# Kernel tuning notes

Measured on AMD Instinct MI355X. Metric: run time of the kernel, lower is better.

The kernel has to match this reference:

```python
import jax, jax.numpy as jnp
import numpy as np

L, H, P = 16384, 1024, 512  # seq len, model width, state size (conj_sym: P = ssm_size//2)
DT_MIN, DT_MAX = 1e-3, 1e-1
STEP_RESCALE = 1.0


def setup_inputs() -> dict:
    key = jax.random.key(0)
    ks = jax.random.split(key, 7)
    input_sequence = jax.random.normal(ks[0], (L, H), dtype=jnp.float32)
    # Lambda: stable diagonal (Re < 0), like DPLR-HiPPO (Re = -0.5, spread imag parts)
    Lambda_re = -0.5 - jax.random.uniform(ks[1], (P,), dtype=jnp.float32)
    Lambda_im = 10.0 * jax.random.normal(ks[2], (P,), dtype=jnp.float32)
    # B (P,H,2) and C (H,P,2): real/imag stacked parameterization
    B = jax.random.normal(ks[3], (P, H, 2), dtype=jnp.float32) / np.float32(np.sqrt(H))
    C = jax.random.normal(ks[4], (H, P, 2), dtype=jnp.float32) / np.float32(np.sqrt(P))
    D = jax.random.normal(ks[5], (H,), dtype=jnp.float32)
    log_step = (jax.random.uniform(ks[6], (P, 1), dtype=jnp.float32)
                * (np.log(DT_MAX) - np.log(DT_MIN)) + np.log(DT_MIN)).astype(jnp.float32)
    return {"input_sequence": input_sequence, "Lambda_re": Lambda_re,
            "Lambda_im": Lambda_im, "B": B, "C": C, "D": D, "log_step": log_step}


def _binop(q_i, q_j):
    # diagonal linear recurrence composition; elementwise, so works on stacked arrays
    A_i, b_i = q_i
    A_j, b_j = q_j
    return (A_j * A_i, A_j * b_i + b_j)


def reference(input_sequence, Lambda_re, Lambda_im, B, C, D, log_step):
    Lambda = Lambda_re + 1j * Lambda_im                      # (P,) complex64
    B_tilde = B[..., 0] + 1j * B[..., 1]                     # (P,H)
    C_tilde = C[..., 0] + 1j * C[..., 1]                     # (H,P)
    Delta = STEP_RESCALE * jnp.exp(log_step[:, 0])           # (P,)
    # ZOH discretization
    Lambda_bar = jnp.exp(Lambda * Delta)                     # (P,)
    B_bar = ((Lambda_bar - 1.0) / Lambda)[:, None] * B_tilde # (P,H)
    # per-step scan elements
    Lambda_elements = jnp.broadcast_to(Lambda_bar, (input_sequence.shape[0], P))
    Bu_elements = jnp.einsum('lh,ph->lp', input_sequence, B_bar)  # (L,P) complex
    _, xs = jax.lax.associative_scan(_binop, (Lambda_elements, Bu_elements))
    # conj_sym readout: 2 * Re(C x)
    ys = 2.0 * jnp.einsum('lp,hp->lh', xs, C_tilde).real     # (L,H) float32
    return ys + input_sequence * D
```

## Files before the change

### kernel.cpp

```cpp
#include <hip/hip_runtime.h>
#include <math.h>

#define LL 16384
#define HH 1024
#define PP 512
#define NP2 1024
#define CHUNK 64
#define NCHUNK 256
#define BM 128
#define BN 128
#define BK 64

typedef unsigned short u16;
typedef __attribute__((ext_vector_type(8))) short bf16x8;
typedef __attribute__((ext_vector_type(4))) float f32x4;

__device__ __forceinline__ u16 f2bf(float f) {
    unsigned u = __float_as_uint(f);
    unsigned r = 0x7fffu + ((u >> 16) & 1u);
    return (u16)((u + r) >> 16);
}
__device__ __forceinline__ float bf2f(u16 x) {
    return __uint_as_float(((unsigned)x) << 16);
}

__device__ __forceinline__ void gload_lds16(const void* g, void* l) {
    __builtin_amdgcn_global_load_lds(
        (const __attribute__((address_space(1))) unsigned int*)g,
        (__attribute__((address_space(3))) unsigned int*)l, 16, 0, 0);
}

__global__ void k_setup(const float* __restrict__ lre, const float* __restrict__ lim,
                        const float* __restrict__ logstep,
                        float* __restrict__ gre, float* __restrict__ gim,
                        float* __restrict__ lbre, float* __restrict__ lbim,
                        float* __restrict__ ltre, float* __restrict__ ltim) {
    int p = threadIdx.x;
    if (p >= PP) return;
    float dt = expf(logstep[p]);
    float ar = lre[p], ai = lim[p];
    float e = expf(ar * dt);
    float s, c;
    sincosf(ai * dt, &s, &c);
    float Lr = e * c, Li = e * s;
    lbre[p] = Lr; lbim[p] = Li;
    float nr = Lr - 1.0f, ni = Li;
    float den = ar * ar + ai * ai;
    gre[p] = (nr * ar + ni * ai) / den;
    gim[p] = (ni * ar - nr * ai) / den;
    float tr = Lr, ti = Li;
    for (int i = 0; i < 6; i++) {
        float rr = tr * tr - ti * ti;
        float mm = 2.0f * tr * ti;
        tr = rr; ti = mm;
    }
    ltre[p] = tr; ltim[p] = ti;
}

__global__ void k_prep2(const float* __restrict__ B,
                        const float* __restrict__ gre, const float* __restrict__ gim,
                        const float* __restrict__ C,
                        u16* __restrict__ bb, u16* __restrict__ cp) {
    if (blockIdx.x < 2048) {
        int t = blockIdx.x * 256 + threadIdx.x;
        int p = t >> 10, h = t & 1023;
        float2 b = ((const float2*)B)[t];
        float gr = gre[p], gi = gim[p];
        bb[(size_t)(2 * p) * HH + h]     = f2bf(gr * b.x - gi * b.y);
        bb[(size_t)(2 * p + 1) * HH + h] = f2bf(gr * b.y + gi * b.x);
    } else {
        int t = (blockIdx.x - 2048) * 256 + threadIdx.x;
        int h = t >> 9, p = t & 511;
        float2 c = ((const float2*)C)[t];
        cp[(size_t)h * NP2 + 2 * p]     = f2bf(c.x);
        cp[(size_t)h * NP2 + 2 * p + 1] = f2bf(-c.y);
    }
}

__global__ void k_cvt(const float* __restrict__ s, u16* __restrict__ d) {
    size_t i = ((size_t)blockIdx.x * 256 + threadIdx.x) * 4;
    float4 v = *(const float4*)&s[i];
    unsigned lo = (unsigned)f2bf(v.x) | ((unsigned)f2bf(v.y) << 16);
    unsigned hi = (unsigned)f2bf(v.z) | ((unsigned)f2bf(v.w) << 16);
    *(uint2*)&d[i] = make_uint2(lo, hi);
}

template<int FUSE>
__global__ __launch_bounds__(256) void k_gemm(
        const u16* __restrict__ A, const u16* __restrict__ Bt,
        void* __restrict__ outp, const int K,
        const u16* __restrict__ ubf, const float* __restrict__ Din,
        const float* __restrict__ lbre, const float* __restrict__ lbim,
        float* __restrict__ frO, float* __restrict__ fiO) {
    __shared__ u16 smem[2 * BM * BK];
    u16* lA = smem;
    u16* lB = smem + BM * BK;
    const int b = blockIdx.x;
    const int xcd = b & 7, s = b >> 3;
    const int m0 = (xcd * 16 + (s >> 3)) * BM;
    const int n0 = (s & 7) * BN;
    const int N = 8 * BN;
    const int t = threadIdx.x;
    const int lane = t & 63, wid = t >> 6;
    const int wm = (wid >> 1) * 64, wn = (wid & 1) * 64;
    const int frow = lane & 15, quad = lane >> 4;
    const int swz = frow & 7;

    f32x4 acc[4][4];
    #pragma unroll
    for (int i = 0; i < 4; i++)
        #pragma unroll
        for (int j = 0; j < 4; j++) acc[i][j] = (f32x4){0.f, 0.f, 0.f, 0.f};

    const int sr = t >> 3, slot = t & 7;
    const int seg = slot ^ (sr & 7);
    const u16* gA = A + (size_t)(m0 + sr) * K + seg * 8;
    const u16* gB = Bt + (size_t)(n0 + sr) * K + seg * 8;
    u16* dA = &lA[sr * BK + slot * 8];
    u16* dB = &lB[sr * BK + slot * 8];

    for (int k0 = 0; k0 < K; k0 += BK) {
        __syncthreads();
        #pragma unroll
        for (int g = 0; g < 4; g++) {
            gload_lds16(gA + (size_t)(32 * g) * K + k0, dA + 32 * g * BK);
            gload_lds16(gB + (size_t)(32 * g) * K + k0, dB + 32 * g * BK);
        }
        __syncthreads();
        #pragma unroll
        for (int kk = 0; kk < 2; kk++) {
            bf16x8 av[4], bv[4];
            #pragma unroll
            for (int i = 0; i < 4; i++)
                av[i] = *(const bf16x8*)&lA[(wm + i * 16 + frow) * BK
                                            + (((kk << 2) | quad) ^ swz) * 8];
            #pragma unroll
            for (int j = 0; j < 4; j++)
                bv[j] = *(const bf16x8*)&lB[(wn + j * 16 + frow) * BK
                                            + (((kk << 2) | quad) ^ swz) * 8];
            #pragma unroll
            for (int i = 0; i < 4; i++)
                #pragma unroll
                for (int j = 0; j < 4; j++)
                    acc[i][j] = __builtin_amdgcn_mfma_f32_16x16x32_bf16(
                        av[i], bv[j], acc[i][j], 0, 0, 0);
        }
    }

    if (FUSE) {
        float* Cout = (float*)outp;
        #pragma unroll
        for (int i = 0; i < 4; i++) {
            const int row = m0 + wm + i * 16 + quad * 4;
            #pragma unroll
            for (int j = 0; j < 4; j++) {
                const int col = n0 + wn + j * 16 + frow;
                const float dv = Din[col];
                f32x4 v = acc[i][j];
                #pragma unroll
                for (int r = 0; r < 4; r++) {
                    const size_t o = (size_t)(row + r) * N + col;
                    Cout[o] = 2.0f * v[r] + bf2f(ubf[o]) * dv;
                }
            }
        }
    } else {
        u16* Cb = (u16*)outp;
        unsigned* sm32 = (unsigned*)smem;
        const int half = wm >> 6;
        const int sq = t & 63, sh = t >> 6;
        const int sp = (n0 >> 1) + sq;
        float sar = 0.f, sai = 0.f, sxr = 0.f, sxi = 0.f;
        if (t < 128) { sar = lbre[sp]; sai = lbim[sp]; }
        __syncthreads();
        #pragma unroll
        for (int i = 0; i < 4; i++) {
            #pragma unroll
            for (int j = 0; j < 4; j++) {
                f32x4 v = acc[i][j];
                #pragma unroll
                for (int r = 0; r < 4; r++)
                    smem[half * 2048 + (quad * 4 + r) * 128 + wn + j * 16 + frow]
                        = f2bf(v[r]);
            }
            __syncthreads();
            #pragma unroll
            for (int c = 0; c < 2; c++) {
                const int fe = (t + c * 256) * 8;
                const int hh = fe >> 11, rem = fe & 2047;
                const int qr = rem >> 7, cb = rem & 127;
                const int row = m0 + hh * 64 + i * 16 + qr;
                *(uint4*)&Cb[(size_t)row * N + n0 + cb] = *(const uint4*)&smem[fe];
            }
            if (t < 128) {
                #pragma unroll
                for (int r = 0; r < 16; r++) {
                    unsigned v = sm32[sh * 1024 + r * 64 + sq];
                    float br = bf2f((u16)(v & 0xffff));
                    float bi = bf2f((u16)(v >> 16));
                    float nr = sar * sxr - sai * sxi + br;
                    float ni = sar * sxi + sai * sxr + bi;
                    sxr = nr; sxi = ni;
                }
            }
            __syncthreads();
        }
        if (t < 128) {
            const int chunk = (m0 >> 6) + sh;
            frO[chunk * PP + sp] = sxr;
            fiO[chunk * PP + sp] = sxi;
        }
    }
}

__global__ __launch_bounds__(256) void k_scan2(
        const float* __restrict__ fr, const float* __restrict__ fi,
        const float* __restrict__ ltre, const float* __restrict__ ltim,
        float* __restrict__ cr, float* __restrict__ ci) {
    __shared__ float Ar[NCHUNK], Ai[NCHUNK], br[NCHUNK], bi[NCHUNK];
    const int p = blockIdx.x;
    const int c = threadIdx.x;
    const float lr = ltre[p], li = ltim[p];
    Ar[c] = lr; Ai[c] = li;
    br[c] = fr[c * PP + p];
    bi[c] = fi[c * PP + p];
    __syncthreads();
    #pragma unroll
    for (int d = 1; d < NCHUNK; d <<= 1) {
        float pAr = 0.f, pAi = 0.f, pbr = 0.f, pbi = 0.f;
        const bool has = (c >= d);
        if (has) { pAr = Ar[c-d]; pAi = Ai[c-d]; pbr = br[c-d]; pbi = bi[c-d]; }
        float cAr = Ar[c], cAi = Ai[c], cbr = br[c], cbi = bi[c];
        __syncthreads();
        if (has) {
            Ar[c] = cAr * pAr - cAi * pAi;
            Ai[c] = cAr * pAi + cAi * pAr;
            br[c] = cAr * pbr - cAi * pbi + cbr;
            bi[c] = cAr * pbi + cAi * pbr + cbi;
        }
        __syncthreads();
    }
    cr[c * PP + p] = (c == 0) ? 0.f : br[c-1];
    ci[c * PP + p] = (c == 0) ? 0.f : bi[c-1];
}

__global__ void k_scan3(unsigned* __restrict__ bu,
                        const float* __restrict__ lbre, const float* __restrict__ lbim,
                        const float* __restrict__ cr, const float* __restrict__ ci) {
    int p = blockIdx.x * 256 + threadIdx.x;
    int c = blockIdx.y;
    float ar = lbre[p], ai = lbim[p];
    float xr = cr[c * PP + p], xi = ci[c * PP + p];
    unsigned* b = bu + (size_t)c * CHUNK * PP + p;
    for (int j = 0; j < CHUNK; j++) {
        unsigned v = *b;
        float br = bf2f((u16)(v & 0xffff));
        float bi = bf2f((u16)(v >> 16));
        float nr = ar * xr - ai * xi + br;
        float ni = ar * xi + ai * xr + bi;
        xr = nr; xi = ni;
        *b = (unsigned)f2bf(xr) | ((unsigned)f2bf(xi) << 16);
        b += PP;
    }
}

extern "C" void kernel_launch(void* const* d_in, const int* in_sizes, int n_in,
                              void* d_out, int out_size, void* d_ws, size_t ws_size,
                              hipStream_t stream) {
    const float* u       = (const float*)d_in[0];
    const float* lre     = (const float*)d_in[1];
    const float* lim     = (const float*)d_in[2];
    const float* B       = (const float*)d_in[3];
    const float* C       = (const float*)d_in[4];
    const float* D       = (const float*)d_in[5];
    const float* logstep = (const float*)d_in[6];
    float* out = (float*)d_out;

    float* w = (float*)d_ws;
    float* gre  = w;
    float* gim  = w + 512;
    float* lbre = w + 1024;
    float* lbim = w + 1536;
    float* ltre = w + 2048;
    float* ltim = w + 2560;
    float* fr   = w + 4096;
    float* fi   = fr + NCHUNK * PP;
    float* cr   = fi + NCHUNK * PP;
    float* ci   = cr + NCHUNK * PP;
    u16*   bub  = (u16*)(w + (1 << 20));
    u16*   ub   = bub + (size_t)LL * NP2;
    u16*   bb   = ub + (size_t)LL * HH;
    u16*   cp   = bb + (size_t)NP2 * HH;

    k_setup<<<1, 512, 0, stream>>>(lre, lim, logstep, gre, gim, lbre, lbim, ltre, ltim);
    k_prep2<<<4096, 256, 0, stream>>>(B, gre, gim, C, bb, cp);
    k_cvt<<<(LL * HH) / 1024, 256, 0, stream>>>(u, ub);
    k_gemm<0><<<(NP2 / BN) * (LL / BM), 256, 0, stream>>>(
        ub, bb, bub, HH, nullptr, nullptr, lbre, lbim, fr, fi);
    k_scan2<<<PP, NCHUNK, 0, stream>>>(fr, fi, ltre, ltim, cr, ci);
    k_scan3<<<dim3(PP / 256, NCHUNK), 256, 0, stream>>>(
        (unsigned*)bub, lbre, lbim, cr, ci);
    k_gemm<1><<<(HH / BN) * (LL / BM), 256, 0, stream>>>(
        bub, cp, out, NP2, ub, D, nullptr, nullptr, nullptr, nullptr);
}
```

Before: 251.6 us.

## Rewrite GEMMs with 256x256 tiles, 4-stage async LDS pipeline, batched scan loads

```diff
diff --git a/kernel.cpp b/kernel.cpp
--- a/kernel.cpp
+++ b/kernel.cpp
@@ -7,9 +7,11 @@
 #define NP2 1024
 #define CHUNK 64
 #define NCHUNK 256
-#define BM 128
-#define BN 128
-#define BK 64
+
+#define BM2 256
+#define BN2 256
+#define SUBK 32
+#define REG_U16 16384
 
 typedef unsigned short u16;
 typedef __attribute__((ext_vector_type(8))) short bf16x8;
@@ -86,71 +88,80 @@
 }
 
 template<int FUSE>
-__global__ __launch_bounds__(256) void k_gemm(
+__global__ __launch_bounds__(512, 2) void k_gemm2(
         const u16* __restrict__ A, const u16* __restrict__ Bt,
         void* __restrict__ outp, const int K,
         const u16* __restrict__ ubf, const float* __restrict__ Din,
         const float* __restrict__ lbre, const float* __restrict__ lbim,
         float* __restrict__ frO, float* __restrict__ fiO) {
-    __shared__ u16 smem[2 * BM * BK];
-    u16* lA = smem;
-    u16* lB = smem + BM * BK;
+    extern __shared__ u16 smem[];
     const int b = blockIdx.x;
-    const int xcd = b & 7, s = b >> 3;
-    const int m0 = (xcd * 16 + (s >> 3)) * BM;
-    const int n0 = (s & 7) * BN;
-    const int N = 8 * BN;
+    const int xcd = b & 7, sidx = b >> 3;
+    const int m0 = (xcd * 8 + (sidx >> 2)) * BM2;
+    const int n0 = (sidx & 3) * BN2;
     const int t = threadIdx.x;
     const int lane = t & 63, wid = t >> 6;
-    const int wm = (wid >> 1) * 64, wn = (wid & 1) * 64;
-    const int frow = lane & 15, quad = lane >> 4;
-    const int swz = frow & 7;
-
-    f32x4 acc[4][4];
+    const int wm = (wid >> 2) * 128, wn = (wid & 3) * 64;
+    const int frow = lane & 15, quad = (lane >> 4) & 3;
+
+    f32x4 acc[8][4];
     #pragma unroll
-    for (int i = 0; i < 4; i++)
+    for (int i = 0; i < 8; i++)
         #pragma unroll
         for (int j = 0; j < 4; j++) acc[i][j] = (f32x4){0.f, 0.f, 0.f, 0.f};
 
-    const int sr = t >> 3, slot = t & 7;
-    const int seg = slot ^ (sr & 7);
+    const int sr = t >> 2, slot = t & 3;
+    const int seg = slot ^ (sr & 3);
     const u16* gA = A + (size_t)(m0 + sr) * K + seg * 8;
     const u16* gB = Bt + (size_t)(n0 + sr) * K + seg * 8;
-    u16* dA = &lA[sr * BK + slot * 8];
-    u16* dB = &lB[sr * BK + slot * 8];
-
-    for (int k0 = 0; k0 < K; k0 += BK) {
-        __syncthreads();
-        #pragma unroll
-        for (int g = 0; g < 4; g++) {
-            gload_lds16(gA + (size_t)(32 * g) * K + k0, dA + 32 * g * BK);
-            gload_lds16(gB + (size_t)(32 * g) * K + k0, dB + 32 * g * BK);
-        }
-        __syncthreads();
-        #pragma unroll
-        for (int kk = 0; kk < 2; kk++) {
-            bf16x8 av[4], bv[4];
-            #pragma unroll
-            for (int i = 0; i < 4; i++)
-                av[i] = *(const bf16x8*)&lA[(wm + i * 16 + frow) * BK
-                                            + (((kk << 2) | quad) ^ swz) * 8];
+    const int ldst = sr * 32 + slot * 8;
+
+    const int aoff = (wm + frow) * 32 + ((quad ^ (frow & 3)) * 8);
+    const int boff = (wn + frow) * 32 + ((quad ^ (frow & 3)) * 8);
+
+    const int NT = K / SUBK;
+
+#define STAGE(k_) do {                                                  \
+        u16* dst_ = smem + ((k_) & 3) * REG_U16 + ldst;                 \
+        const u16* ga_ = gA + (k_) * SUBK;                              \
+        const u16* gb_ = gB + (k_) * SUBK;                              \
+        gload_lds16(ga_,                   dst_);                       \
+        gload_lds16(ga_ + (size_t)128 * K, dst_ + 4096);                \
+        gload_lds16(gb_,                   dst_ + 8192);                \
+        gload_lds16(gb_ + (size_t)128 * K, dst_ + 12288);               \
+    } while (0)
+
+    STAGE(0); STAGE(1); STAGE(2);
+
+    for (int s = 0; s < NT; ++s) {
+        if (s + 3 < NT) STAGE(s + 3);
+        if (s < NT - 2)       asm volatile("s_waitcnt vmcnt(8)" ::: "memory");
+        else if (s == NT - 2) asm volatile("s_waitcnt vmcnt(4)" ::: "memory");
+        else                  asm volatile("s_waitcnt vmcnt(0)" ::: "memory");
+        asm volatile("s_barrier" ::: "memory");
+        const u16* Ar = smem + (s & 3) * REG_U16;
+        const u16* Br = Ar + 8192;
+        bf16x8 av[8], bv[4];
+        #pragma unroll
+        for (int i = 0; i < 8; i++) av[i] = *(const bf16x8*)&Ar[aoff + i * 512];
+        #pragma unroll
+        for (int j = 0; j < 4; j++) bv[j] = *(const bf16x8*)&Br[boff + j * 512];
+        __builtin_amdgcn_s_setprio(1);
+        #pragma unroll
+        for (int i = 0; i < 8; i++)
             #pragma unroll
             for (int j = 0; j < 4; j++)
-                bv[j] = *(const bf16x8*)&lB[(wn + j * 16 + frow) * BK
-                                            + (((kk << 2) | quad) ^ swz) * 8];
-            #pragma unroll
-            for (int i = 0; i < 4; i++)
-                #pragma unroll
-                for (int j = 0; j < 4; j++)
-                    acc[i][j] = __builtin_amdgcn_mfma_f32_16x16x32_bf16(
-                        av[i], bv[j], acc[i][j], 0, 0, 0);
-        }
-    }
+                acc[i][j] = __builtin_amdgcn_mfma_f32_16x16x32_bf16(
+                    av[i], bv[j], acc[i][j], 0, 0, 0);
+        __builtin_amdgcn_s_setprio(0);
+        asm volatile("s_barrier" ::: "memory");
+    }
+#undef STAGE
 
     if (FUSE) {
         float* Cout = (float*)outp;
         #pragma unroll
-        for (int i = 0; i < 4; i++) {
+        for (int i = 0; i < 8; i++) {
             const int row = m0 + wm + i * 16 + quad * 4;
             #pragma unroll
             for (int j = 0; j < 4; j++) {
@@ -159,7 +170,7 @@
                 f32x4 v = acc[i][j];
                 #pragma unroll
                 for (int r = 0; r < 4; r++) {
-                    const size_t o = (size_t)(row + r) * N + col;
+                    const size_t o = (size_t)(row + r) * 1024 + col;
                     Cout[o] = 2.0f * v[r] + bf2f(ubf[o]) * dv;
                 }
             }
@@ -167,49 +178,39 @@
     } else {
         u16* Cb = (u16*)outp;
         unsigned* sm32 = (unsigned*)smem;
-        const int half = wm >> 6;
-        const int sq = t & 63, sh = t >> 6;
-        const int sp = (n0 >> 1) + sq;
-        float sar = 0.f, sai = 0.f, sxr = 0.f, sxi = 0.f;
-        if (t < 128) { sar = lbre[sp]; sai = lbim[sp]; }
-        __syncthreads();
-        #pragma unroll
-        for (int i = 0; i < 4; i++) {
+        #pragma unroll
+        for (int i = 0; i < 8; i++)
             #pragma unroll
             for (int j = 0; j < 4; j++) {
                 f32x4 v = acc[i][j];
                 #pragma unroll
                 for (int r = 0; r < 4; r++)
-                    smem[half * 2048 + (quad * 4 + r) * 128 + wn + j * 16 + frow]
+                    smem[(wm + i * 16 + quad * 4 + r) * 256 + wn + j * 16 + frow]
                         = f2bf(v[r]);
             }
-            __syncthreads();
-            #pragma unroll
-            for (int c = 0; c < 2; c++) {
-                const int fe = (t + c * 256) * 8;
-                const int hh = fe >> 11, rem = fe & 2047;
-                const int qr = rem >> 7, cb = rem & 127;
-                const int row = m0 + hh * 64 + i * 16 + qr;
-                *(uint4*)&Cb[(size_t)row * N + n0 + cb] = *(const uint4*)&smem[fe];
-            }
-            if (t < 128) {
-                #pragma unroll
-                for (int r = 0; r < 16; r++) {
-                    unsigned v = sm32[sh * 1024 + r * 64 + sq];
-                    float br = bf2f((u16)(v & 0xffff));
-                    float bi = bf2f((u16)(v >> 16));
-                    float nr = sar * sxr - sai * sxi + br;
-                    float ni = sar * sxi + sai * sxr + bi;
-                    sxr = nr; sxi = ni;
-                }
-            }
-            __syncthreads();
-        }
-        if (t < 128) {
-            const int chunk = (m0 >> 6) + sh;
-            frO[chunk * PP + sp] = sxr;
-            fiO[chunk * PP + sp] = sxi;
-        }
+        __syncthreads();
+        #pragma unroll
+        for (int k = 0; k < 16; k++) {
+            const int l = t + k * 512;
+            const int row = l >> 5, c16 = (l & 31) * 8;
+            *(uint4*)&Cb[(size_t)(m0 + row) * 1024 + n0 + c16] =
+                ((const uint4*)smem)[l];
+        }
+        const int ch = t >> 7, q = t & 127;
+        const int sp = (n0 >> 1) + q;
+        const float sar = lbre[sp], sai = lbim[sp];
+        float xr = 0.f, xi = 0.f;
+        #pragma unroll 8
+        for (int r = 0; r < 64; r++) {
+            unsigned v = sm32[(ch * 64 + r) * 128 + q];
+            float br = bf2f((u16)(v & 0xffff));
+            float bi = bf2f((u16)(v >> 16));
+            float nr = sar * xr - sai * xi + br;
+            float ni = sar * xi + sai * xr + bi;
+            xr = nr; xi = ni;
+        }
+        frO[((m0 >> 6) + ch) * PP + sp] = xr;
+        fiO[((m0 >> 6) + ch) * PP + sp] = xi;
     }
 }
 
@@ -252,15 +253,21 @@
     float ar = lbre[p], ai = lbim[p];
     float xr = cr[c * PP + p], xi = ci[c * PP + p];
     unsigned* b = bu + (size_t)c * CHUNK * PP + p;
-    for (int j = 0; j < CHUNK; j++) {
-        unsigned v = *b;
-        float br = bf2f((u16)(v & 0xffff));
-        float bi = bf2f((u16)(v >> 16));
-        float nr = ar * xr - ai * xi + br;
-        float ni = ar * xi + ai * xr + bi;
-        xr = nr; xi = ni;
-        *b = (unsigned)f2bf(xr) | ((unsigned)f2bf(xi) << 16);
-        b += PP;
+    for (int j = 0; j < CHUNK; j += 4) {
+        unsigned vv[4];
+        vv[0] = b[0]; vv[1] = b[PP]; vv[2] = b[2 * PP]; vv[3] = b[3 * PP];
+        unsigned w[4];
+        #pragma unroll
+        for (int q = 0; q < 4; q++) {
+            float br = bf2f((u16)(vv[q] & 0xffff));
+            float bi = bf2f((u16)(vv[q] >> 16));
+            float nr = ar * xr - ai * xi + br;
+            float ni = ar * xi + ai * xr + bi;
+            xr = nr; xi = ni;
+            w[q] = (unsigned)f2bf(xr) | ((unsigned)f2bf(xi) << 16);
+        }
+        b[0] = w[0]; b[PP] = w[1]; b[2 * PP] = w[2]; b[3 * PP] = w[3];
+        b += 4 * PP;
     }
 }
 
@@ -292,14 +299,23 @@
     u16*   bb   = ub + (size_t)LL * HH;
     u16*   cp   = bb + (size_t)NP2 * HH;
 
+    static int attr_done = 0;
+    if (!attr_done) {
+        hipFuncSetAttribute(reinterpret_cast<const void*>(k_gemm2<0>),
+                            hipFuncAttributeMaxDynamicSharedMemorySize, 131072);
+        hipFuncSetAttribute(reinterpret_cast<const void*>(k_gemm2<1>),
+                            hipFuncAttributeMaxDynamicSharedMemorySize, 131072);
+        attr_done = 1;
+    }
+
     k_setup<<<1, 512, 0, stream>>>(lre, lim, logstep, gre, gim, lbre, lbim, ltre, ltim);
     k_prep2<<<4096, 256, 0, stream>>>(B, gre, gim, C, bb, cp);
     k_cvt<<<(LL * HH) / 1024, 256, 0, stream>>>(u, ub);
-    k_gemm<0><<<(NP2 / BN) * (LL / BM), 256, 0, stream>>>(
+    k_gemm2<0><<<(NP2 / BN2) * (LL / BM2), 512, 131072, stream>>>(
         ub, bb, bub, HH, nullptr, nullptr, lbre, lbim, fr, fi);
     k_scan2<<<PP, NCHUNK, 0, stream>>>(fr, fi, ltre, ltim, cr, ci);
     k_scan3<<<dim3(PP / 256, NCHUNK), 256, 0, stream>>>(
         (unsigned*)bub, lbre, lbim, cr, ci);
-    k_gemm<1><<<(HH / BN) * (LL / BM), 256, 0, stream>>>(
+    k_gemm2<1><<<(HH / BN2) * (LL / BM2), 512, 131072, stream>>>(
         bub, cp, out, NP2, ub, D, nullptr, nullptr, nullptr, nullptr);
 }
```

Measured after the change: 244.7 us. 1.03x faster.
